# Kernel tuning notes

Measured on AMD Instinct MI355X. Metric: run time of the kernel, lower is better.

Reference implementation:

```python
import jax, jax.numpy as jnp
import numpy as np

B, LQ, S, D, H = 8, 1024, 256, 1024, 16
HD = D // H
LN_EPS = 1e-5


def layer_norm(x, g, b):
    m = jnp.mean(x, axis=-1, keepdims=True)
    v = jnp.mean((x - m) ** 2, axis=-1, keepdims=True)
    return (x - m) / jnp.sqrt(v + LN_EPS) * g + b


def setup_inputs() -> dict:
    key = jax.random.key(0)
    ks = jax.random.split(key, 12)
    sc = 0.02
    p = lambda k, shp: jax.random.normal(k, shp, dtype=jnp.float32) * sc
    return {
        "memory": jax.random.normal(ks[0], (B, LQ, D // 2), dtype=jnp.float32),
        "gaze_features": jax.random.normal(ks[1], (B, LQ, D // 2), dtype=jnp.float32),
        "text_features": jax.random.normal(ks[2], (B, S, D), dtype=jnp.float32),
        "w_in": p(ks[3], (3 * D, D)),  # packed q,k,v in_proj (torch MHA layout)
        "b_in": jnp.zeros((3 * D,), jnp.float32),
        "w_o": p(ks[4], (D, D)),
        "b_o": jnp.zeros((D,), jnp.float32),
        "w1": p(ks[5], (D, D)),
        "b1": jnp.zeros((D,), jnp.float32),
        "w2": p(ks[6], (D, D)),
        "b2": jnp.zeros((D,), jnp.float32),
        "g1": jnp.ones((D,), jnp.float32),
        "be1": jnp.zeros((D,), jnp.float32),
        "g2": jnp.ones((D,), jnp.float32),
        "be2": jnp.zeros((D,), jnp.float32),
    }


def reference(memory, gaze_features, text_features, w_in, b_in, w_o, b_o,
              w1, b1, w2, b2, g1, be1, g2, be2):
    combined = jnp.concatenate([memory, gaze_features], axis=-1)  # [B, LQ, D]
    wq, wk, wv = w_in[:D], w_in[D:2 * D], w_in[2 * D:]
    bq, bk, bv = b_in[:D], b_in[D:2 * D], b_in[2 * D:]

    q = (combined @ wq.T + bq).reshape(B, LQ, H, HD)
    k = (text_features @ wk.T + bk).reshape(B, S, H, HD)
    v = (text_features @ wv.T + bv).reshape(B, S, H, HD)

    scores = jnp.einsum("bqhd,bkhd->bhqk", q, k) / jnp.sqrt(jnp.float32(HD))
    attn_w = jax.nn.softmax(scores, axis=-1)
    ctx = jnp.einsum("bhqk,bkhd->bqhd", attn_w, v).reshape(B, LQ, D)
    attn_output = ctx @ w_o.T + b_o  # [B, LQ, D]

    # dual FFN branches share linear1/linear2 (as in the source); dropout = eval identity
    ffn = jax.nn.relu(attn_output @ w1.T + b1) @ w2.T + b2
    refpoint_embed = layer_norm(ffn, g1, be1)
    tgt = layer_norm(ffn, g2, be2)

    # vectorized box decode (replaces the per-element Python loop)
    s = jax.nn.sigmoid(attn_output[..., :4])
    xc, yc, w, h = s[..., 0], s[..., 1], s[..., 2], s[..., 3]
    init_box_proposal = jnp.stack(
        [xc - w / 2, yc - h / 2, xc + w / 2, yc + h / 2], axis=-1)  # [B, LQ, 4]

    return refpoint_embed, tgt, init_box_proposal
```

## Files before the change

kernel.cpp:

```cpp
#include <hip/hip_runtime.h>


typedef unsigned short u16;
typedef unsigned int u32;
typedef __bf16 bf16x8 __attribute__((ext_vector_type(8)));
typedef float f32x4 __attribute__((ext_vector_type(4)));
typedef u16 u16x4 __attribute__((ext_vector_type(4)));

struct CvtArgs { const void* in[15]; };

__device__ __forceinline__ u16 f2bf(float f) {
  u32 u = __builtin_bit_cast(u32, f);
  u += 0x7fffu + ((u >> 16) & 1u);
  return (u16)(u >> 16);
}
__device__ __forceinline__ float bf2f(u16 h) {
  u32 u = ((u32)h) << 16;
  return __builtin_bit_cast(float, u);
}

struct WsPtrs {
  u16 *c_mem, *c_gaze, *c_text, *c_win, *c_bin, *c_wo, *c_bo, *c_w1, *c_b1,
      *c_w2, *c_b2, *c_g1, *c_be1, *c_g2, *c_be2;
  u16 *q, *k, *v, *ctx, *woT, *wf, *bfb, *h1, *ffnb;
};
__device__ __forceinline__ WsPtrs wsp(u16* C) {
  WsPtrs w;
  w.c_mem = C;                 w.c_gaze = C + 4194304;   w.c_text = C + 8388608;
  w.c_win = C + 10485760;      w.c_bin = C + 13631488;   w.c_wo = C + 13634560;
  w.c_bo = C + 14683136;       w.c_w1 = C + 14684160;    w.c_b1 = C + 15732736;
  w.c_w2 = C + 15733760;       w.c_b2 = C + 16782336;    w.c_g1 = C + 16783360;
  w.c_be1 = C + 16784384;      w.c_g2 = C + 16785408;    w.c_be2 = C + 16786432;
  u16* B2 = C + 16787488;
  w.q = B2;                    w.k = B2 + 8388608;       w.v = B2 + 10485760;
  w.ctx = B2 + 12582912;
  w.woT = B2 + 20971520;
  w.wf  = B2 + 22020096;
  w.bfb = B2 + 23068672;
  w.h1  = B2 + 29360128;
  w.ffnb = B2;
  return w;
}

__device__ __forceinline__ void cvt_chunk(bool f32in, u16* dst,
                                          const void* const* srcs, u32 c8) {
  const u32 cum[16] = {0u, 4194304u, 8388608u, 10485760u, 13631488u, 13634560u,
                       14683136u, 14684160u, 15732736u, 15733760u, 16782336u,
                       16783360u, 16784384u, 16785408u, 16786432u, 16787456u};
  u32 base = c8 * 8u;
  int idx = 0;
#pragma unroll
  for (int i = 1; i < 15; ++i) if (base >= cum[i]) idx = i;
  u32 off = base - cum[idx];
  if (f32in) {
    const float* s = (const float*)srcs[idx] + off;
    float4 a = ((const float4*)s)[0];
    float4 b = ((const float4*)s)[1];
    u16 t[8] = {f2bf(a.x), f2bf(a.y), f2bf(a.z), f2bf(a.w),
                f2bf(b.x), f2bf(b.y), f2bf(b.z), f2bf(b.w)};
    *(uint4*)(dst + base) = *(const uint4*)t;
  } else {
    *(uint4*)(dst + base) = *(const uint4*)((const u16*)srcs[idx] + off);
  }
}

__global__ __launch_bounds__(256) void cvt_tr(CvtArgs a, u16* ws) {
  __shared__ u16 tile[128 * 136];
  const bool f32in = (((const u32*)a.in[11])[0] == 0x3F800000u);
  const int bid = blockIdx.x, tid = threadIdx.x;
  if (bid < 64) {
    WsPtrs w = wsp(ws);
    int tr = bid >> 3, tc = bid & 7;
#pragma unroll
    for (int p = 0; p < 8; ++p) {
      int t = p * 16 + (tid >> 4);
      int j8 = (tid & 15) * 8;
      u16 tmp[8];
      if (f32in) {
        const float* s = (const float*)a.in[5] + (size_t)(tr * 128 + t) * 1024 + tc * 128 + j8;
        float4 x = ((const float4*)s)[0], y = ((const float4*)s)[1];
        tmp[0]=f2bf(x.x); tmp[1]=f2bf(x.y); tmp[2]=f2bf(x.z); tmp[3]=f2bf(x.w);
        tmp[4]=f2bf(y.x); tmp[5]=f2bf(y.y); tmp[6]=f2bf(y.z); tmp[7]=f2bf(y.w);
      } else {
        *(uint4*)tmp = *(const uint4*)((const u16*)a.in[5] + (size_t)(tr * 128 + t) * 1024 + tc * 128 + j8);
      }
      *(uint4*)&tile[t * 136 + j8] = *(const uint4*)tmp;
    }
    __syncthreads();
#pragma unroll
    for (int p = 0; p < 8; ++p) {
      int j = p * 16 + (tid >> 4);
      int t8 = (tid & 15) * 8;
      u16 tmp[8];
#pragma unroll
      for (int i = 0; i < 8; ++i) tmp[i] = tile[(t8 + i) * 136 + j];
      *(uint4*)(w.woT + (size_t)(tc * 128 + j) * 1024 + tr * 128 + t8) = *(const uint4*)tmp;
    }
  } else {
    u32 c8 = (u32)(bid - 64) * 256u + tid;
    if (c8 < 2098432u) cvt_chunk(f32in, ws, a.in, c8);
  }
}

__device__ __forceinline__ void stage_half(
    u16* dst, const u16* P0, const u16* P1, int Ksplit, int ld0, int ld1,
    int rowbase, int k0, int tid) {
#pragma unroll
  for (int r = 0; r < 2; ++r) {
    int p = (r << 9) + tid;
    int rr = p >> 3;
    int gk = k0 + ((((p & 7) ^ (rr & 7))) << 3);
    const u16* src = (gk < Ksplit)
        ? P0 + (size_t)(rowbase + rr) * ld0 + gk
        : P1 + (size_t)(rowbase + rr) * ld1 + (gk - Ksplit);
    __builtin_amdgcn_global_load_lds(
        (const __attribute__((address_space(1))) void*)src,
        (__attribute__((address_space(3))) void*)(dst + ((size_t)p << 3)),
        16, 0, 0);
  }
}

__device__ __forceinline__ void gemm256(
    u16* lds,
    const u16* A0, const u16* A1, int Ksplit, int lda0, int lda1,
    const u16* W, const u16* bias, u16* out, int N, int K,
    int mode, int lg, int m0, int n0) {
  const int tid = threadIdx.x;
  const int lane = tid & 63;
  const int quad = lane >> 4, l16 = lane & 15;
  const int wave = tid >> 6;
  const int wm = wave >> 2, wn = wave & 3;
  const int BIGK = 0x40000000;
  const int NT = K >> 6;

  u16* sA0b = lds;
  u16* sB0b = lds + 32768;

  f32x4 acc[2][4][2][2];
#pragma unroll
  for (int h = 0; h < 2; ++h)
#pragma unroll
    for (int i = 0; i < 4; ++i)
#pragma unroll
      for (int g = 0; g < 2; ++g)
#pragma unroll
        for (int j = 0; j < 2; ++j)
          acc[h][i][g][j] = (f32x4){0.f, 0.f, 0.f, 0.f};

  stage_half(sA0b,        A0, A1, Ksplit, lda0, lda1, m0,       0, tid);
  stage_half(sB0b,        W,  W,  BIGK,   K,    K,    n0,       0, tid);
  stage_half(sB0b + 8192, W,  W,  BIGK,   K,    K,    n0 + 128, 0, tid);
  stage_half(sA0b + 8192, A0, A1, Ksplit, lda0, lda1, m0 + 128, 0, tid);
  asm volatile("s_waitcnt vmcnt(4)" ::: "memory");
  __builtin_amdgcn_s_barrier();
  __builtin_amdgcn_sched_barrier(0);

  for (int T = 0; T < NT; ++T) {
    u16* sAc = lds + ((T & 1) << 14);
    u16* sBc = lds + 32768 + ((T & 1) << 14);
    u16* sAn = lds + (((T + 1) & 1) << 14);
    u16* sBn = lds + 32768 + (((T + 1) & 1) << 14);
    const bool more = (T + 1 < NT);
    const int k0n = (T + 1) << 6;
#pragma unroll
    for (int p = 0; p < 4; ++p) {
      const int h = p >> 1, g = p & 1;
      bf16x8 af[4][2], bw[2][2];
#pragma unroll
      for (int i = 0; i < 4; ++i) {
        const int rr = wm * 64 + i * 16 + l16;
        const int sw = rr & 7;
#pragma unroll
        for (int ks = 0; ks < 2; ++ks)
          af[i][ks] = *(const bf16x8*)(sAc + (h << 13) + (rr << 6) + (((ks * 4 + quad) ^ sw) << 3));
      }
#pragma unroll
      for (int j = 0; j < 2; ++j) {
        const int rr = wn * 32 + j * 16 + l16;
        const int sw = rr & 7;
#pragma unroll
        for (int ks = 0; ks < 2; ++ks)
          bw[j][ks] = *(const bf16x8*)(sBc + (g << 13) + (rr << 6) + (((ks * 4 + quad) ^ sw) << 3));
      }
      if (more && p == 0) {
        stage_half(sAn, A0, A1, Ksplit, lda0, lda1, m0, k0n, tid);
        stage_half(sBn, W, W, BIGK, K, K, n0, k0n, tid);
      }
      if (more && p == 1) {
        stage_half(sBn + 8192, W, W, BIGK, K, K, n0 + 128, k0n, tid);
        stage_half(sAn + 8192, A0, A1, Ksplit, lda0, lda1, m0 + 128, k0n, tid);
      }
      __builtin_amdgcn_s_barrier();
      __builtin_amdgcn_sched_barrier(0);
      __builtin_amdgcn_s_setprio(1);
#pragma unroll
      for (int i = 0; i < 4; ++i)
#pragma unroll
        for (int j = 0; j < 2; ++j)
#pragma unroll
          for (int ks = 0; ks < 2; ++ks)
            acc[h][i][g][j] = __builtin_amdgcn_mfma_f32_16x16x32_bf16(
                af[i][ks], bw[j][ks], acc[h][i][g][j], 0, 0, 0);
      __builtin_amdgcn_s_setprio(0);
      if (p == 0) {
        if (more) asm volatile("s_waitcnt vmcnt(4)" ::: "memory");
        else      asm volatile("s_waitcnt vmcnt(0)" ::: "memory");
      }
      if (p == 3 && more) asm volatile("s_waitcnt vmcnt(4)" ::: "memory");
      __builtin_amdgcn_s_barrier();
      __builtin_amdgcn_sched_barrier(0);
    }
  }

#pragma unroll
  for (int h = 0; h < 2; ++h)
#pragma unroll
    for (int i = 0; i < 4; ++i)
#pragma unroll
      for (int g = 0; g < 2; ++g)
#pragma unroll
        for (int j = 0; j < 2; ++j) {
          const int n = n0 + g * 128 + wn * 32 + j * 16 + l16;
          const float bv = bias ? bf2f(bias[n]) : 0.f;
#pragma unroll
          for (int rr4 = 0; rr4 < 4; ++rr4) {
            const int m = m0 + h * 128 + wm * 64 + i * 16 + quad * 4 + rr4;
            float val = acc[h][i][g][j][rr4] + bv;
            if (mode == 1) val = fmaxf(val, 0.f);
            if (mode <= 1) {
              out[(size_t)m * N + n] = f2bf(val);
            } else if (mode == 3) {
              int b = m >> lg, l = m & ((1 << lg) - 1);
              int hh = n >> 6, d = n & 63;
              out[((size_t)(b * 16 + hh) << (lg + 6)) + ((size_t)l << 6) + d] = f2bf(val);
            } else {
              int b = m >> lg, s = m & ((1 << lg) - 1);
              int hh = n >> 6, d = n & 63;
              out[((size_t)(((b * 16 + hh) << 6) + d) << lg) + s] = f2bf(val);
            }
          }
        }
}

__global__ __launch_bounds__(512, 2) void qkvwf(u16* ws) {
  __shared__ __align__(16) u16 lds[65536];
  WsPtrs w = wsp(ws);
  const int bid = blockIdx.x, tid = threadIdx.x;
  if (bid >= 208) {
    int i = (bid - 208) * 512 + tid;
    const u16* w1row = w.c_w1 + (size_t)i * 1024;
    float acc = bf2f(w.c_b1[i]);
    for (int kk = 0; kk < 1024; kk += 8) {
      bf16x8 wv = *(const bf16x8*)(w1row + kk);
      bf16x8 bv = *(const bf16x8*)(w.c_bo + kk);
#pragma unroll
      for (int j = 0; j < 8; ++j) acc += (float)wv[j] * (float)bv[j];
    }
    w.bfb[i] = f2bf(acc);
    return;
  }
  const u16 *A0, *A1, *W, *bias; u16* out;
  int Ksplit, lda0, lda1, mode, lg, m0, n0;
  if (bid < 128) {
    A0 = w.c_mem; A1 = w.c_gaze; Ksplit = 512; lda0 = 512; lda1 = 512;
    W = w.c_win; bias = w.c_bin; out = w.q; mode = 3; lg = 10;
    m0 = (bid >> 2) * 256; n0 = (bid & 3) * 256;
  } else if (bid < 160) {
    int u = bid - 128;
    A0 = w.c_text; A1 = w.c_text; Ksplit = 1024; lda0 = 1024; lda1 = 1024;
    W = w.c_win + 1048576; bias = w.c_bin + 1024; out = w.k; mode = 3; lg = 8;
    m0 = (u >> 2) * 256; n0 = (u & 3) * 256;
  } else if (bid < 192) {
    int u = bid - 160;
    A0 = w.c_text; A1 = w.c_text; Ksplit = 1024; lda0 = 1024; lda1 = 1024;
    W = w.c_win + 2097152; bias = w.c_bin + 2048; out = w.v; mode = 4; lg = 8;
    m0 = (u >> 2) * 256; n0 = (u & 3) * 256;
  } else {
    int u = bid - 192;
    A0 = w.c_w1; A1 = w.c_w1; Ksplit = 1024; lda0 = 1024; lda1 = 1024;
    W = w.woT; bias = nullptr; out = w.wf; mode = 0; lg = 0;
    m0 = (u >> 2) * 256; n0 = (u & 3) * 256;
  }
  gemm256(lds, A0, A1, Ksplit, lda0, lda1, W, bias, out, 1024, 1024,
          mode, lg, m0, n0);
}

__global__ __launch_bounds__(256) void attn_kernel(u16* ws) {
  __shared__ u16 sV[64 * 256];
  __shared__ u16 sKP[256 * 64];
  WsPtrs w = wsp(ws);
  const int tid = threadIdx.x;
  const int wave = tid >> 6, lane = tid & 63;
  const int quad = lane >> 4, l16 = lane & 15;
  const int qb = blockIdx.x & 15, bh = blockIdx.x >> 4;

  {
    int rr = tid >> 3, c8 = (tid & 7) << 3;
    const u16* kb = w.k + (size_t)bh * 16384;
#pragma unroll
    for (int p = 0; p < 8; ++p) {
      int row = p * 32 + rr;
      uint4 val = *(const uint4*)(kb + row * 64 + c8);
      *(uint4*)&sKP[(row << 6) + ((((c8 >> 3) ^ (row & 7))) << 3)] = val;
    }
    int r2 = tid >> 5, c8b = (tid & 31) << 3;
    const u16* vb = w.v + (size_t)bh * 16384;
#pragma unroll
    for (int p = 0; p < 8; ++p) {
      int row = p * 8 + r2;
      uint4 val = *(const uint4*)(vb + (row << 8) + c8b);
      *(uint4*)&sV[(row << 8) + ((((c8b >> 3) ^ (row & 7))) << 3)] = val;
    }
  }
  bf16x8 aq[2];
  {
    const u16* qrow = w.q + ((size_t)bh * 1024 + qb * 64 + wave * 16 + l16) * 64 + quad * 8;
    aq[0] = *(const bf16x8*)(qrow);
    aq[1] = *(const bf16x8*)(qrow + 32);
  }
  __syncthreads();

  f32x4 sc[16];
#pragma unroll
  for (int nt = 0; nt < 16; ++nt) sc[nt] = (f32x4){0.f, 0.f, 0.f, 0.f};
#pragma unroll
  for (int ks = 0; ks < 2; ++ks) {
    const int ch = (ks << 2) + quad;
#pragma unroll
    for (int nt = 0; nt < 16; ++nt) {
      int row = nt * 16 + l16;
      bf16x8 bk = *(const bf16x8*)&sKP[(row << 6) + ((ch ^ (row & 7)) << 3)];
      sc[nt] = __builtin_amdgcn_mfma_f32_16x16x32_bf16(aq[ks], bk, sc[nt], 0, 0, 0);
    }
  }
#pragma unroll
  for (int rr = 0; rr < 4; ++rr) {
    float mx = -1e30f;
#pragma unroll
    for (int nt = 0; nt < 16; ++nt) mx = fmaxf(mx, sc[nt][rr]);
    for (int off = 1; off < 16; off <<= 1) mx = fmaxf(mx, __shfl_xor(mx, off, 64));
    float sum = 0.f;
#pragma unroll
    for (int nt = 0; nt < 16; ++nt) {
      float p = __expf((sc[nt][rr] - mx) * 0.125f);
      sc[nt][rr] = p; sum += p;
    }
    for (int off = 1; off < 16; off <<= 1) sum += __shfl_xor(sum, off, 64);
    float inv = 1.f / sum;
#pragma unroll
    for (int nt = 0; nt < 16; ++nt) sc[nt][rr] *= inv;
  }
  __syncthreads();
#pragma unroll
  for (int nt = 0; nt < 16; ++nt)
#pragma unroll
    for (int rr = 0; rr < 4; ++rr) {
      int row = wave * 16 + quad * 4 + rr;
      int col = nt * 16 + l16;
      sKP[(row << 8) + (((col >> 3) ^ (row & 7)) << 3) + (col & 7)] = f2bf(sc[nt][rr]);
    }
  __syncthreads();

  f32x4 o[4];
#pragma unroll
  for (int j = 0; j < 4; ++j) o[j] = (f32x4){0.f, 0.f, 0.f, 0.f};
#pragma unroll
  for (int ks = 0; ks < 8; ++ks) {
    const int ch = (ks << 2) + quad;
    int prow = wave * 16 + l16;
    bf16x8 ap = *(const bf16x8*)&sKP[(prow << 8) + ((ch ^ (prow & 7)) << 3)];
#pragma unroll
    for (int j = 0; j < 4; ++j) {
      int vrow = j * 16 + l16;
      bf16x8 bv = *(const bf16x8*)&sV[(vrow << 8) + ((ch ^ (vrow & 7)) << 3)];
      o[j] = __builtin_amdgcn_mfma_f32_16x16x32_bf16(ap, bv, o[j], 0, 0, 0);
    }
  }
  const int b = bh >> 4, h = bh & 15;
#pragma unroll
  for (int j = 0; j < 4; ++j)
#pragma unroll
    for (int rr = 0; rr < 4; ++rr) {
      int m = qb * 64 + wave * 16 + quad * 4 + rr;
      int d = h * 64 + j * 16 + l16;
      w.ctx[((size_t)b * 1024 + m) * 1024 + d] = f2bf(o[j][rr]);
    }
}

__global__ __launch_bounds__(512, 2) void h1box(u16* ws, void* out, const void* g1orig) {
  __shared__ __align__(16) u16 lds[65536];
  WsPtrs w = wsp(ws);
  const int u = blockIdx.x, tid = threadIdx.x;
  {
    const bool f32out = (((const u32*)g1orig)[0] == 0x3F800000u);
    int m = u * 64 + (tid >> 3);
    int l8 = tid & 7;
    int k0 = l8 * 128;
    const u16* crow = w.ctx + (size_t)m * 1024 + k0;
    float a0 = 0.f, a1 = 0.f, a2 = 0.f, a3 = 0.f;
#pragma unroll
    for (int kk = 0; kk < 128; kk += 8) {
      bf16x8 cv = *(const bf16x8*)(crow + kk);
      bf16x8 w0 = *(const bf16x8*)(w.c_wo + k0 + kk);
      bf16x8 w1v = *(const bf16x8*)(w.c_wo + 1024 + k0 + kk);
      bf16x8 w2v = *(const bf16x8*)(w.c_wo + 2048 + k0 + kk);
      bf16x8 w3v = *(const bf16x8*)(w.c_wo + 3072 + k0 + kk);
#pragma unroll
      for (int j = 0; j < 8; ++j) {
        float c = (float)cv[j];
        a0 += c * (float)w0[j]; a1 += c * (float)w1v[j];
        a2 += c * (float)w2v[j]; a3 += c * (float)w3v[j];
      }
    }
    for (int off = 1; off < 8; off <<= 1) {
      a0 += __shfl_xor(a0, off, 64); a1 += __shfl_xor(a1, off, 64);
      a2 += __shfl_xor(a2, off, 64); a3 += __shfl_xor(a3, off, 64);
    }
    if (l8 == 0) {
      a0 += bf2f(w.c_bo[0]); a1 += bf2f(w.c_bo[1]);
      a2 += bf2f(w.c_bo[2]); a3 += bf2f(w.c_bo[3]);
      float s0 = 1.f / (1.f + __expf(-a0)), s1 = 1.f / (1.f + __expf(-a1));
      float s2 = 1.f / (1.f + __expf(-a2)), s3 = 1.f / (1.f + __expf(-a3));
      float o0 = s0 - s2 * 0.5f, o1 = s1 - s3 * 0.5f;
      float o2 = s0 + s2 * 0.5f, o3 = s1 + s3 * 0.5f;
      if (f32out) {
        float* fo = (float*)out + 16777216;
        *(float4*)(fo + (size_t)m * 4) = make_float4(o0, o1, o2, o3);
      } else {
        u16* bo = (u16*)out + 16777216;
        u16x4 o; o[0] = f2bf(o0); o[1] = f2bf(o1); o[2] = f2bf(o2); o[3] = f2bf(o3);
        *(u16x4*)(bo + (size_t)m * 4) = o;
      }
    }
  }
  gemm256(lds, w.ctx, w.ctx, 0x40000000, 1024, 1024, w.wf, w.bfb, w.h1,
          1024, 1024, 1, 0, (u >> 2) * 256, (u & 3) * 256);
}

__global__ __launch_bounds__(512, 2) void w2gemm(u16* ws) {
  __shared__ __align__(16) u16 lds[65536];
  WsPtrs w = wsp(ws);
  gemm256(lds, w.h1, w.h1, 0x40000000, 1024, 1024, w.c_w2, w.c_b2, w.ffnb,
          1024, 1024, 0, 0, (blockIdx.x >> 2) * 256, (blockIdx.x & 3) * 256);
}

__global__ __launch_bounds__(256) void ln_kernel(u16* ws, void* outv, const void* g1orig) {
  WsPtrs w = wsp(ws);
  const bool f32out = (((const u32*)g1orig)[0] == 0x3F800000u);
  const int row = blockIdx.x, tid = threadIdx.x;
  int c = tid * 4;
  u16x4 xr = *(const u16x4*)(w.ffnb + (size_t)row * 1024 + c);
  float x[4] = {bf2f(xr[0]), bf2f(xr[1]), bf2f(xr[2]), bf2f(xr[3])};
  float s = x[0] + x[1] + x[2] + x[3];
  float s2 = x[0]*x[0] + x[1]*x[1] + x[2]*x[2] + x[3]*x[3];
  for (int m = 32; m >= 1; m >>= 1) { s += __shfl_xor(s, m, 64); s2 += __shfl_xor(s2, m, 64); }
  __shared__ float red[8];
  int wv = tid >> 6;
  if ((tid & 63) == 0) { red[wv] = s; red[4 + wv] = s2; }
  __syncthreads();
  s = red[0] + red[1] + red[2] + red[3];
  s2 = red[4] + red[5] + red[6] + red[7];
  float mean = s * (1.f / 1024.f);
  float var = s2 * (1.f / 1024.f) - mean * mean;
  float inv = rsqrtf(var + 1e-5f);
  float y[4] = {(x[0] - mean) * inv, (x[1] - mean) * inv, (x[2] - mean) * inv, (x[3] - mean) * inv};
  float v1[4], v2[4];
#pragma unroll
  for (int i = 0; i < 4; ++i) {
    v1[i] = y[i] * bf2f(w.c_g1[c + i]) + bf2f(w.c_be1[c + i]);
    v2[i] = y[i] * bf2f(w.c_g2[c + i]) + bf2f(w.c_be2[c + i]);
  }
  if (f32out) {
    float* fo = (float*)outv;
    *(float4*)(fo + (size_t)row * 1024 + c) = make_float4(v1[0], v1[1], v1[2], v1[3]);
    *(float4*)(fo + 8388608 + (size_t)row * 1024 + c) = make_float4(v2[0], v2[1], v2[2], v2[3]);
  } else {
    u16* out = (u16*)outv;
    u16x4 o1, o2;
#pragma unroll
    for (int i = 0; i < 4; ++i) { o1[i] = f2bf(v1[i]); o2[i] = f2bf(v2[i]); }
    *(u16x4*)(out + (size_t)row * 1024 + c) = o1;
    *(u16x4*)(out + 8388608 + (size_t)row * 1024 + c) = o2;
  }
}

extern "C" void kernel_launch(void* const* d_in, const int* in_sizes, int n_in,
                              void* d_out, int out_size, void* d_ws, size_t ws_size,
                              hipStream_t stream) {
  CvtArgs ca;
  for (int i = 0; i < 15; ++i) ca.in[i] = d_in[i];
  u16* ws = (u16*)d_ws;
  cvt_tr<<<dim3(8261), dim3(256), 0, stream>>>(ca, ws);
  qkvwf<<<dim3(210), dim3(512), 0, stream>>>(ws);
  attn_kernel<<<dim3(2048), dim3(256), 0, stream>>>(ws);
  h1box<<<dim3(128), dim3(512), 0, stream>>>(ws, d_out, d_in[11]);
  w2gemm<<<dim3(128), dim3(512), 0, stream>>>(ws);
  ln_kernel<<<dim3(8192), dim3(256), 0, stream>>>(ws, d_out, d_in[11]);
}
```

Measured before the change: 340.1 us.

## Reorder GEMM subtile sweep to reuse A/B fragments across quadrants

Replaces the four-phase (h,g) loop, which reloaded both A and B fragments from LDS on every phase, with a serpentine order (A0B0, A0B1, A1B1, A1B0) that keeps one operand in registers between phases and reloads only the other. Global-to-LDS staging is spread over three phases, and the vmcnt waits are retuned to match. The LDS destination offset is computed from a wave-uniform readfirstlane base so it stays scalar. The aim is fewer LDS reads per K step; the waitcnt retuning is easy to get wrong and could cause races or stalls.

```diff
diff --git a/kernel.cpp b/kernel.cpp
--- a/kernel.cpp
+++ b/kernel.cpp
@@ -104,7 +104,7 @@
 
 __device__ __forceinline__ void stage_half(
     u16* dst, const u16* P0, const u16* P1, int Ksplit, int ld0, int ld1,
-    int rowbase, int k0, int tid) {
+    int rowbase, int k0, int tid, int wb) {
 #pragma unroll
   for (int r = 0; r < 2; ++r) {
     int p = (r << 9) + tid;
@@ -113,10 +113,10 @@
     const u16* src = (gk < Ksplit)
         ? P0 + (size_t)(rowbase + rr) * ld0 + gk
         : P1 + (size_t)(rowbase + rr) * ld1 + (gk - Ksplit);
+    u16* d = dst + (((size_t)((r << 9) + wb)) << 3);
     __builtin_amdgcn_global_load_lds(
         (const __attribute__((address_space(1))) void*)src,
-        (__attribute__((address_space(3))) void*)(dst + ((size_t)p << 3)),
-        16, 0, 0);
+        (__attribute__((address_space(3))) void*)d, 16, 0, 0);
   }
 }
 
@@ -130,12 +130,10 @@
   const int quad = lane >> 4, l16 = lane & 15;
   const int wave = tid >> 6;
   const int wm = wave >> 2, wn = wave & 3;
+  const int wb = __builtin_amdgcn_readfirstlane(tid & 448);
   const int BIGK = 0x40000000;
   const int NT = K >> 6;
 
-  u16* sA0b = lds;
-  u16* sB0b = lds + 32768;
-
   f32x4 acc[2][4][2][2];
 #pragma unroll
   for (int h = 0; h < 2; ++h)
@@ -147,13 +145,15 @@
         for (int j = 0; j < 2; ++j)
           acc[h][i][g][j] = (f32x4){0.f, 0.f, 0.f, 0.f};
 
-  stage_half(sA0b,        A0, A1, Ksplit, lda0, lda1, m0,       0, tid);
-  stage_half(sB0b,        W,  W,  BIGK,   K,    K,    n0,       0, tid);
-  stage_half(sB0b + 8192, W,  W,  BIGK,   K,    K,    n0 + 128, 0, tid);
-  stage_half(sA0b + 8192, A0, A1, Ksplit, lda0, lda1, m0 + 128, 0, tid);
+  stage_half(lds,                 A0, A1, Ksplit, lda0, lda1, m0,       0, tid, wb);
+  stage_half(lds + 32768,         W,  W,  BIGK,   K,    K,    n0,       0, tid, wb);
+  stage_half(lds + 32768 + 8192,  W,  W,  BIGK,   K,    K,    n0 + 128, 0, tid, wb);
+  stage_half(lds + 8192,          A0, A1, Ksplit, lda0, lda1, m0 + 128, 0, tid, wb);
   asm volatile("s_waitcnt vmcnt(4)" ::: "memory");
   __builtin_amdgcn_s_barrier();
   __builtin_amdgcn_sched_barrier(0);
+
+  bf16x8 af[4][2], bw[2][2];
 
   for (int T = 0; T < NT; ++T) {
     u16* sAc = lds + ((T & 1) << 14);
@@ -162,54 +162,109 @@
     u16* sBn = lds + 32768 + (((T + 1) & 1) << 14);
     const bool more = (T + 1 < NT);
     const int k0n = (T + 1) << 6;
-#pragma unroll
-    for (int p = 0; p < 4; ++p) {
-      const int h = p >> 1, g = p & 1;
-      bf16x8 af[4][2], bw[2][2];
-#pragma unroll
-      for (int i = 0; i < 4; ++i) {
-        const int rr = wm * 64 + i * 16 + l16;
-        const int sw = rr & 7;
-#pragma unroll
-        for (int ks = 0; ks < 2; ++ks)
-          af[i][ks] = *(const bf16x8*)(sAc + (h << 13) + (rr << 6) + (((ks * 4 + quad) ^ sw) << 3));
-      }
-#pragma unroll
-      for (int j = 0; j < 2; ++j) {
-        const int rr = wn * 32 + j * 16 + l16;
-        const int sw = rr & 7;
-#pragma unroll
-        for (int ks = 0; ks < 2; ++ks)
-          bw[j][ks] = *(const bf16x8*)(sBc + (g << 13) + (rr << 6) + (((ks * 4 + quad) ^ sw) << 3));
-      }
-      if (more && p == 0) {
-        stage_half(sAn, A0, A1, Ksplit, lda0, lda1, m0, k0n, tid);
-        stage_half(sBn, W, W, BIGK, K, K, n0, k0n, tid);
-      }
-      if (more && p == 1) {
-        stage_half(sBn + 8192, W, W, BIGK, K, K, n0 + 128, k0n, tid);
-        stage_half(sAn + 8192, A0, A1, Ksplit, lda0, lda1, m0 + 128, k0n, tid);
-      }
-      __builtin_amdgcn_s_barrier();
-      __builtin_amdgcn_sched_barrier(0);
-      __builtin_amdgcn_s_setprio(1);
+
+#pragma unroll
+    for (int i = 0; i < 4; ++i) {
+      const int rr = wm * 64 + i * 16 + l16;
+      const int sw = rr & 7;
+#pragma unroll
+      for (int ks = 0; ks < 2; ++ks)
+        af[i][ks] = *(const bf16x8*)(sAc + (rr << 6) + (((ks * 4 + quad) ^ sw) << 3));
+    }
+#pragma unroll
+    for (int j = 0; j < 2; ++j) {
+      const int rr = wn * 32 + j * 16 + l16;
+      const int sw = rr & 7;
+#pragma unroll
+      for (int ks = 0; ks < 2; ++ks)
+        bw[j][ks] = *(const bf16x8*)(sBc + (rr << 6) + (((ks * 4 + quad) ^ sw) << 3));
+    }
+    if (more) {
+      stage_half(sAn, A0, A1, Ksplit, lda0, lda1, m0, k0n, tid, wb);
+      stage_half(sBn, W, W, BIGK, K, K, n0, k0n, tid, wb);
+    }
+    __builtin_amdgcn_s_setprio(1);
+#pragma unroll
+    for (int ks = 0; ks < 2; ++ks)
 #pragma unroll
       for (int i = 0; i < 4; ++i)
 #pragma unroll
         for (int j = 0; j < 2; ++j)
-#pragma unroll
-          for (int ks = 0; ks < 2; ++ks)
-            acc[h][i][g][j] = __builtin_amdgcn_mfma_f32_16x16x32_bf16(
-                af[i][ks], bw[j][ks], acc[h][i][g][j], 0, 0, 0);
-      __builtin_amdgcn_s_setprio(0);
-      if (p == 0) {
-        if (more) asm volatile("s_waitcnt vmcnt(4)" ::: "memory");
-        else      asm volatile("s_waitcnt vmcnt(0)" ::: "memory");
-      }
-      if (p == 3 && more) asm volatile("s_waitcnt vmcnt(4)" ::: "memory");
-      __builtin_amdgcn_s_barrier();
-      __builtin_amdgcn_sched_barrier(0);
-    }
+          acc[0][i][0][j] = __builtin_amdgcn_mfma_f32_16x16x32_bf16(
+              af[i][ks], bw[j][ks], acc[0][i][0][j], 0, 0, 0);
+    __builtin_amdgcn_s_setprio(0);
+    if (more) asm volatile("s_waitcnt vmcnt(6)" ::: "memory");
+    else      asm volatile("s_waitcnt vmcnt(2)" ::: "memory");
+    __builtin_amdgcn_s_barrier();
+    __builtin_amdgcn_sched_barrier(0);
+
+#pragma unroll
+    for (int j = 0; j < 2; ++j) {
+      const int rr = wn * 32 + j * 16 + l16;
+      const int sw = rr & 7;
+#pragma unroll
+      for (int ks = 0; ks < 2; ++ks)
+        bw[j][ks] = *(const bf16x8*)(sBc + 8192 + (rr << 6) + (((ks * 4 + quad) ^ sw) << 3));
+    }
+    if (more) stage_half(sBn + 8192, W, W, BIGK, K, K, n0 + 128, k0n, tid, wb);
+    __builtin_amdgcn_s_setprio(1);
+#pragma unroll
+    for (int ks = 0; ks < 2; ++ks)
+#pragma unroll
+      for (int i = 0; i < 4; ++i)
+#pragma unroll
+        for (int j = 0; j < 2; ++j)
+          acc[0][i][1][j] = __builtin_amdgcn_mfma_f32_16x16x32_bf16(
+              af[i][ks], bw[j][ks], acc[0][i][1][j], 0, 0, 0);
+    __builtin_amdgcn_s_setprio(0);
+    if (more) asm volatile("s_waitcnt vmcnt(6)" ::: "memory");
+    else      asm volatile("s_waitcnt vmcnt(0)" ::: "memory");
+    __builtin_amdgcn_s_barrier();
+    __builtin_amdgcn_sched_barrier(0);
+
+#pragma unroll
+    for (int i = 0; i < 4; ++i) {
+      const int rr = wm * 64 + i * 16 + l16;
+      const int sw = rr & 7;
+#pragma unroll
+      for (int ks = 0; ks < 2; ++ks)
+        af[i][ks] = *(const bf16x8*)(sAc + 8192 + (rr << 6) + (((ks * 4 + quad) ^ sw) << 3));
+    }
+    if (more) stage_half(sAn + 8192, A0, A1, Ksplit, lda0, lda1, m0 + 128, k0n, tid, wb);
+    __builtin_amdgcn_s_setprio(1);
+#pragma unroll
+    for (int ks = 0; ks < 2; ++ks)
+#pragma unroll
+      for (int i = 0; i < 4; ++i)
+#pragma unroll
+        for (int j = 0; j < 2; ++j)
+          acc[1][i][1][j] = __builtin_amdgcn_mfma_f32_16x16x32_bf16(
+              af[i][ks], bw[j][ks], acc[1][i][1][j], 0, 0, 0);
+    __builtin_amdgcn_s_setprio(0);
+    __builtin_amdgcn_s_barrier();
+    __builtin_amdgcn_sched_barrier(0);
+
+#pragma unroll
+    for (int j = 0; j < 2; ++j) {
+      const int rr = wn * 32 + j * 16 + l16;
+      const int sw = rr & 7;
+#pragma unroll
+      for (int ks = 0; ks < 2; ++ks)
+        bw[j][ks] = *(const bf16x8*)(sBc + (rr << 6) + (((ks * 4 + quad) ^ sw) << 3));
+    }
+    __builtin_amdgcn_s_setprio(1);
+#pragma unroll
+    for (int ks = 0; ks < 2; ++ks)
+#pragma unroll
+      for (int i = 0; i < 4; ++i)
+#pragma unroll
+        for (int j = 0; j < 2; ++j)
+          acc[1][i][0][j] = __builtin_amdgcn_mfma_f32_16x16x32_bf16(
+              af[i][ks], bw[j][ks], acc[1][i][0][j], 0, 0, 0);
+    __builtin_amdgcn_s_setprio(0);
+    if (more) asm volatile("s_waitcnt vmcnt(4)" ::: "memory");
+    __builtin_amdgcn_s_barrier();
+    __builtin_amdgcn_sched_barrier(0);
   }
 
 #pragma unroll
```

Result: faster. 315.9 us (-7.1%).
